# Performance work log

Measured on AMD Instinct MI355X. Metric: run time of the kernel, lower is better.

Reference implementation:

```python
import jax, jax.numpy as jnp
import numpy as np

IN_FEATURES = 4096
OUT_FEATURES = 4096
LORA_R = 64
LORA_ALPHA = 16
SCALING = LORA_ALPHA / LORA_R  # 0.25


def setup_inputs() -> dict:
    key = jax.random.key(0)
    k_x, k_w, k_s, k_a, k_b = jax.random.split(key, 5)
    x = jax.random.normal(k_x, (4, 2048, IN_FEATURES), dtype=jnp.float32)
    # int8 quantized base weight in [-8, 7] as in the torch buffer init
    weight_quantized = jax.random.randint(k_w, (OUT_FEATURES, IN_FEATURES), -8, 7, dtype=jnp.int8)
    weight_scale = jax.random.normal(k_s, (1,), dtype=jnp.float32)
    lora_A = jax.random.normal(k_a, (LORA_R, IN_FEATURES), dtype=jnp.float32) * 0.01
    # torch init is zeros; use small random values so the LoRA path is exercised
    lora_B = jax.random.normal(k_b, (OUT_FEATURES, LORA_R), dtype=jnp.float32) * 0.01
    return {"x": x, "weight_quantized": weight_quantized, "weight_scale": weight_scale,
            "lora_A": lora_A, "lora_B": lora_B}


def reference(x, weight_quantized, weight_scale, lora_A, lora_B):
    # 1. dequantize base weight on the fly: [out, in]
    w_dequant = weight_quantized.astype(x.dtype) * weight_scale
    # 2. base GEMM: [B, S, in] x [in, out] -> [B, S, out]
    base = jnp.einsum('bsi,oi->bso', x, w_dequant)
    # 3. LoRA low-rank update (dropout is identity in eval mode)
    lora = jnp.einsum('bsr,or->bso', jnp.einsum('bsi,ri->bsr', x, lora_A), lora_B)
    return base + lora * SCALING
```

## Files before the change

### kernel.cpp

```cpp
#include <hip/hip_runtime.h>

#define M_TOT 8192
#define K_TOT 4096
#define N_TOT 4096
#define RANK  64
#define SCALING 0.25f

typedef __bf16 bf16x8 __attribute__((ext_vector_type(8)));
typedef float floatx4 __attribute__((ext_vector_type(4)));

static __device__ __forceinline__ unsigned short f32_to_bf16(float f) {
  unsigned int u = __float_as_uint(f);
  u += 0x7FFFu + ((u >> 16) & 1u);
  return (unsigned short)(u >> 16);
}

static __device__ __forceinline__ void async_ld16(const void* g, void* l) {
  __builtin_amdgcn_global_load_lds(
      (const __attribute__((address_space(1))) unsigned int*)g,
      (__attribute__((address_space(3))) unsigned int*)l, 16, 0, 0);
}

__global__ __launch_bounds__(256) void cvt_x_kernel(const float4* __restrict__ x,
                                                    ushort4* __restrict__ xb) {
  int i = blockIdx.x * 256 + threadIdx.x;
  float4 v = x[i];
  ushort4 o;
  o.x = f32_to_bf16(v.x);
  o.y = f32_to_bf16(v.y);
  o.z = f32_to_bf16(v.z);
  o.w = f32_to_bf16(v.w);
  xb[i] = o;
}

__global__ __launch_bounds__(256) void build_weff_kernel(
    const int* __restrict__ wq, const float* __restrict__ scale_p,
    const float* __restrict__ A, const float* __restrict__ B,
    unsigned short* __restrict__ Weff) {
  __shared__ float Bs[64][65];
  __shared__ float As[64][65];

  const int tid = threadIdx.x;
  const int o0 = blockIdx.y * 64;
  const int k0 = blockIdx.x * 64;
  const float scale = scale_p[0];

  for (int i = tid; i < 64 * 64; i += 256) {
    int o = i >> 6, r = i & 63;
    Bs[o][r] = B[(size_t)(o0 + o) * RANK + r];
  }
  for (int i = tid; i < 64 * 64; i += 256) {
    int r = i >> 6, kk = i & 63;
    As[r][kk] = A[(size_t)r * K_TOT + k0 + kk];
  }
  __syncthreads();

  const int to = tid >> 4;
  const int tk = tid & 15;
  float acc[4][4] = {};
#pragma unroll 8
  for (int r = 0; r < RANK; ++r) {
    float bv[4], av[4];
#pragma unroll
    for (int a = 0; a < 4; ++a) bv[a] = Bs[to * 4 + a][r];
#pragma unroll
    for (int b = 0; b < 4; ++b) av[b] = As[r][tk * 4 + b];
#pragma unroll
    for (int a = 0; a < 4; ++a)
#pragma unroll
      for (int b = 0; b < 4; ++b) acc[a][b] += bv[a] * av[b];
  }
#pragma unroll
  for (int a = 0; a < 4; ++a) {
    const int o = o0 + to * 4 + a;
    const size_t base = (size_t)o * K_TOT + k0 + tk * 4;
    const int4 wv = *(const int4*)(wq + base);
    ushort4 st;
    st.x = f32_to_bf16((float)wv.x * scale + SCALING * acc[a][0]);
    st.y = f32_to_bf16((float)wv.y * scale + SCALING * acc[a][1]);
    st.z = f32_to_bf16((float)wv.z * scale + SCALING * acc[a][2]);
    st.w = f32_to_bf16((float)wv.w * scale + SCALING * acc[a][3]);
    *(ushort4*)(Weff + base) = st;
  }
}

__global__ __launch_bounds__(256) void gemm_kernel(
    const unsigned short* __restrict__ Xb,
    const unsigned short* __restrict__ Wb,
    float* __restrict__ out) {
  __shared__ __align__(16) unsigned short As[2 * 128 * 32];
  __shared__ __align__(16) unsigned short Bs[2 * 128 * 32];

  const int tid = threadIdx.x;
  const int lane = tid & 63;
  const int wave = tid >> 6;
  const int wm = wave >> 1;
  const int wn = wave & 1;

  const int bM = blockIdx.y * 128;
  const int bN = blockIdx.x * 128;

  const int sRow = tid >> 2;
  const int sCol = (tid & 3) * 8;
  const unsigned short* xg0 = Xb + (size_t)(bM + sRow) * K_TOT + sCol;
  const unsigned short* xg1 = xg0 + (size_t)64 * K_TOT;
  const unsigned short* wg0 = Wb + (size_t)(bN + sRow) * K_TOT + sCol;
  const unsigned short* wg1 = wg0 + (size_t)64 * K_TOT;
  unsigned short* la00 = As + tid * 8;
  unsigned short* la01 = As + 64 * 32 + tid * 8;
  unsigned short* la10 = As + 128 * 32 + tid * 8;
  unsigned short* la11 = As + 128 * 32 + 64 * 32 + tid * 8;
  unsigned short* lb00 = Bs + tid * 8;
  unsigned short* lb01 = Bs + 64 * 32 + tid * 8;
  unsigned short* lb10 = Bs + 128 * 32 + tid * 8;
  unsigned short* lb11 = Bs + 128 * 32 + 64 * 32 + tid * 8;

  const unsigned short* pa = As + ((wm * 64) + (lane & 15)) * 32 + (lane >> 4) * 8;
  const unsigned short* pb = Bs + ((wn * 64) + (lane & 15)) * 32 + (lane >> 4) * 8;

  floatx4 acc[4][4] = {};

  for (int kt = 0; kt < K_TOT; kt += 64) {
    __syncthreads();
    async_ld16(xg0 + kt, la00);
    async_ld16(xg1 + kt, la01);
    async_ld16(xg0 + kt + 32, la10);
    async_ld16(xg1 + kt + 32, la11);
    async_ld16(wg0 + kt, lb00);
    async_ld16(wg1 + kt, lb01);
    async_ld16(wg0 + kt + 32, lb10);
    async_ld16(wg1 + kt + 32, lb11);
    __syncthreads();

#pragma unroll
    for (int ks = 0; ks < 2; ++ks) {
      const unsigned short* pak = pa + ks * 128 * 32;
      const unsigned short* pbk = pb + ks * 128 * 32;
      bf16x8 af[4], bf[4];
#pragma unroll
      for (int i = 0; i < 4; ++i) af[i] = *(const bf16x8*)(pak + i * 16 * 32);
#pragma unroll
      for (int j = 0; j < 4; ++j) bf[j] = *(const bf16x8*)(pbk + j * 16 * 32);
#pragma unroll
      for (int i = 0; i < 4; ++i)
#pragma unroll
        for (int j = 0; j < 4; ++j)
          acc[i][j] = __builtin_amdgcn_mfma_f32_16x16x32_bf16(af[i], bf[j], acc[i][j], 0, 0, 0);
    }
  }

  const int row0 = bM + wm * 64 + ((lane >> 4) << 2);
  const int col0 = bN + wn * 64 + (lane & 15);
#pragma unroll
  for (int i = 0; i < 4; ++i) {
#pragma unroll
    for (int j = 0; j < 4; ++j) {
#pragma unroll
      for (int r = 0; r < 4; ++r) {
        out[(size_t)(row0 + i * 16 + r) * N_TOT + (col0 + j * 16)] = acc[i][j][r];
      }
    }
  }
}

extern "C" void kernel_launch(void* const* d_in, const int* in_sizes, int n_in,
                              void* d_out, int out_size, void* d_ws, size_t ws_size,
                              hipStream_t stream) {
  const float* x      = (const float*)d_in[0];
  const int*   wq     = (const int*)d_in[1];
  const float* wscale = (const float*)d_in[2];
  const float* lora_A = (const float*)d_in[3];
  const float* lora_B = (const float*)d_in[4];
  float* out = (float*)d_out;

  unsigned short* xb   = (unsigned short*)d_ws;
  unsigned short* weff = (unsigned short*)((char*)d_ws + (size_t)M_TOT * K_TOT * 2);

  cvt_x_kernel<<<32768, 256, 0, stream>>>((const float4*)x, (ushort4*)xb);
  build_weff_kernel<<<dim3(K_TOT / 64, N_TOT / 64), 256, 0, stream>>>(
      wq, wscale, lora_A, lora_B, weff);
  gemm_kernel<<<dim3(N_TOT / 128, M_TOT / 128), 256, 0, stream>>>(xb, weff, out);
}
```

Baseline: 596.3 us.

## Compute LoRA as separate low-rank path instead of folding into dequantized weight

The LoRA update is no longer folded into a dense effective weight through a scalar-FMA B@A product. A prep kernel now dequantizes the weight and converts A and the pre-scaled B to bf16. A new MFMA kernel computes Y = X·Aᵀ, and the main GEMM adds one extra K=64 step of Y·Bᵀ before writing out. This removes the dense rank-64 outer-product work per weight element, but adds a second full pass over X in a kernel launched with only 128 blocks, which may be latency bound.

```diff
diff --git a/kernel.cpp b/kernel.cpp
--- a/kernel.cpp
+++ b/kernel.cpp
@@ -33,60 +33,100 @@
   xb[i] = o;
 }
 
-__global__ __launch_bounds__(256) void build_weff_kernel(
+__global__ __launch_bounds__(256) void prep_kernel(
     const int* __restrict__ wq, const float* __restrict__ scale_p,
     const float* __restrict__ A, const float* __restrict__ B,
-    unsigned short* __restrict__ Weff) {
-  __shared__ float Bs[64][65];
-  __shared__ float As[64][65];
-
+    unsigned short* __restrict__ Weff, unsigned short* __restrict__ Ab,
+    unsigned short* __restrict__ Bb) {
+  const int blk = blockIdx.x;
   const int tid = threadIdx.x;
-  const int o0 = blockIdx.y * 64;
-  const int k0 = blockIdx.x * 64;
-  const float scale = scale_p[0];
-
-  for (int i = tid; i < 64 * 64; i += 256) {
-    int o = i >> 6, r = i & 63;
-    Bs[o][r] = B[(size_t)(o0 + o) * RANK + r];
-  }
-  for (int i = tid; i < 64 * 64; i += 256) {
-    int r = i >> 6, kk = i & 63;
-    As[r][kk] = A[(size_t)r * K_TOT + k0 + kk];
-  }
-  __syncthreads();
-
-  const int to = tid >> 4;
-  const int tk = tid & 15;
-  float acc[4][4] = {};
-#pragma unroll 8
-  for (int r = 0; r < RANK; ++r) {
-    float bv[4], av[4];
-#pragma unroll
-    for (int a = 0; a < 4; ++a) bv[a] = Bs[to * 4 + a][r];
-#pragma unroll
-    for (int b = 0; b < 4; ++b) av[b] = As[r][tk * 4 + b];
-#pragma unroll
-    for (int a = 0; a < 4; ++a)
-#pragma unroll
-      for (int b = 0; b < 4; ++b) acc[a][b] += bv[a] * av[b];
-  }
-#pragma unroll
-  for (int a = 0; a < 4; ++a) {
-    const int o = o0 + to * 4 + a;
-    const size_t base = (size_t)o * K_TOT + k0 + tk * 4;
-    const int4 wv = *(const int4*)(wq + base);
+  if (blk < 16384) {
+    const float scale = scale_p[0];
+    const size_t i = (size_t)(blk * 256 + tid) * 4;
+    const int4 wv = *(const int4*)(wq + i);
     ushort4 st;
-    st.x = f32_to_bf16((float)wv.x * scale + SCALING * acc[a][0]);
-    st.y = f32_to_bf16((float)wv.y * scale + SCALING * acc[a][1]);
-    st.z = f32_to_bf16((float)wv.z * scale + SCALING * acc[a][2]);
-    st.w = f32_to_bf16((float)wv.w * scale + SCALING * acc[a][3]);
-    *(ushort4*)(Weff + base) = st;
-  }
+    st.x = f32_to_bf16((float)wv.x * scale);
+    st.y = f32_to_bf16((float)wv.y * scale);
+    st.z = f32_to_bf16((float)wv.z * scale);
+    st.w = f32_to_bf16((float)wv.w * scale);
+    *(ushort4*)(Weff + i) = st;
+  } else if (blk < 16640) {
+    const size_t i = (size_t)((blk - 16384) * 256 + tid) * 4;
+    const float4 v = *(const float4*)(A + i);
+    ushort4 st;
+    st.x = f32_to_bf16(v.x);
+    st.y = f32_to_bf16(v.y);
+    st.z = f32_to_bf16(v.z);
+    st.w = f32_to_bf16(v.w);
+    *(ushort4*)(Ab + i) = st;
+  } else {
+    const size_t i = (size_t)((blk - 16640) * 256 + tid) * 4;
+    const float4 v = *(const float4*)(B + i);
+    ushort4 st;
+    st.x = f32_to_bf16(v.x * SCALING);
+    st.y = f32_to_bf16(v.y * SCALING);
+    st.z = f32_to_bf16(v.z * SCALING);
+    st.w = f32_to_bf16(v.w * SCALING);
+    *(ushort4*)(Bb + i) = st;
+  }
+}
+
+__global__ __launch_bounds__(256) void lora_y_kernel(
+    const unsigned short* __restrict__ Xb,
+    const unsigned short* __restrict__ Ab,
+    unsigned short* __restrict__ Yb) {
+  __shared__ __align__(16) unsigned short Xs[2 * 64 * 32];
+  __shared__ __align__(16) unsigned short As[2 * 64 * 32];
+
+  const int tid = threadIdx.x;
+  const int lane = tid & 63;
+  const int wave = tid >> 6;
+  const int m0 = blockIdx.x * 64;
+
+  const int sRow = tid >> 2;
+  const int sCol = (tid & 3) * 8;
+  const unsigned short* xg = Xb + (size_t)(m0 + sRow) * K_TOT + sCol;
+  const unsigned short* ag = Ab + (size_t)sRow * K_TOT + sCol;
+  unsigned short* lx0 = Xs + tid * 8;
+  unsigned short* lx1 = Xs + 64 * 32 + tid * 8;
+  unsigned short* la0 = As + tid * 8;
+  unsigned short* la1 = As + 64 * 32 + tid * 8;
+
+  const unsigned short* px = Xs + (wave * 16 + (lane & 15)) * 32 + (lane >> 4) * 8;
+  const unsigned short* pav = As + (lane & 15) * 32 + (lane >> 4) * 8;
+
+  floatx4 acc[4] = {};
+  for (int kt = 0; kt < K_TOT; kt += 64) {
+    __syncthreads();
+    async_ld16(xg + kt, lx0);
+    async_ld16(xg + kt + 32, lx1);
+    async_ld16(ag + kt, la0);
+    async_ld16(ag + kt + 32, la1);
+    __syncthreads();
+#pragma unroll
+    for (int ks = 0; ks < 2; ++ks) {
+      bf16x8 xf = *(const bf16x8*)(px + ks * 64 * 32);
+#pragma unroll
+      for (int j = 0; j < 4; ++j) {
+        bf16x8 af = *(const bf16x8*)(pav + ks * 64 * 32 + j * 16 * 32);
+        acc[j] = __builtin_amdgcn_mfma_f32_16x16x32_bf16(xf, af, acc[j], 0, 0, 0);
+      }
+    }
+  }
+  const int row0 = m0 + wave * 16 + ((lane >> 4) << 2);
+  const int col0 = lane & 15;
+#pragma unroll
+  for (int j = 0; j < 4; ++j)
+#pragma unroll
+    for (int r = 0; r < 4; ++r)
+      Yb[(size_t)(row0 + r) * RANK + (col0 + j * 16)] = f32_to_bf16(acc[j][r]);
 }
 
 __global__ __launch_bounds__(256) void gemm_kernel(
     const unsigned short* __restrict__ Xb,
     const unsigned short* __restrict__ Wb,
+    const unsigned short* __restrict__ Yb,
+    const unsigned short* __restrict__ Bb,
     float* __restrict__ out) {
   __shared__ __align__(16) unsigned short As[2 * 128 * 32];
   __shared__ __align__(16) unsigned short Bs[2 * 128 * 32];
@@ -149,18 +189,47 @@
     }
   }
 
+  {
+    const unsigned short* yg0 = Yb + (size_t)(bM + sRow) * RANK + sCol;
+    const unsigned short* yg1 = yg0 + (size_t)64 * RANK;
+    const unsigned short* bg0 = Bb + (size_t)(bN + sRow) * RANK + sCol;
+    const unsigned short* bg1 = bg0 + (size_t)64 * RANK;
+    __syncthreads();
+    async_ld16(yg0, la00);
+    async_ld16(yg1, la01);
+    async_ld16(yg0 + 32, la10);
+    async_ld16(yg1 + 32, la11);
+    async_ld16(bg0, lb00);
+    async_ld16(bg1, lb01);
+    async_ld16(bg0 + 32, lb10);
+    async_ld16(bg1 + 32, lb11);
+    __syncthreads();
+#pragma unroll
+    for (int ks = 0; ks < 2; ++ks) {
+      const unsigned short* pak = pa + ks * 128 * 32;
+      const unsigned short* pbk = pb + ks * 128 * 32;
+      bf16x8 af[4], bf[4];
+#pragma unroll
+      for (int i = 0; i < 4; ++i) af[i] = *(const bf16x8*)(pak + i * 16 * 32);
+#pragma unroll
+      for (int j = 0; j < 4; ++j) bf[j] = *(const bf16x8*)(pbk + j * 16 * 32);
+#pragma unroll
+      for (int i = 0; i < 4; ++i)
+#pragma unroll
+        for (int j = 0; j < 4; ++j)
+          acc[i][j] = __builtin_amdgcn_mfma_f32_16x16x32_bf16(af[i], bf[j], acc[i][j], 0, 0, 0);
+    }
+  }
+
   const int row0 = bM + wm * 64 + ((lane >> 4) << 2);
   const int col0 = bN + wn * 64 + (lane & 15);
 #pragma unroll
-  for (int i = 0; i < 4; ++i) {
-#pragma unroll
-    for (int j = 0; j < 4; ++j) {
-#pragma unroll
-      for (int r = 0; r < 4; ++r) {
+  for (int i = 0; i < 4; ++i)
+#pragma unroll
+    for (int j = 0; j < 4; ++j)
+#pragma unroll
+      for (int r = 0; r < 4; ++r)
         out[(size_t)(row0 + i * 16 + r) * N_TOT + (col0 + j * 16)] = acc[i][j][r];
-      }
-    }
-  }
 }
 
 extern "C" void kernel_launch(void* const* d_in, const int* in_sizes, int n_in,
@@ -173,11 +242,15 @@
   const float* lora_B = (const float*)d_in[4];
   float* out = (float*)d_out;
 
-  unsigned short* xb   = (unsigned short*)d_ws;
-  unsigned short* weff = (unsigned short*)((char*)d_ws + (size_t)M_TOT * K_TOT * 2);
+  char* ws = (char*)d_ws;
+  unsigned short* xb   = (unsigned short*)(ws);
+  unsigned short* weff = (unsigned short*)(ws + 67108864);
+  unsigned short* yb   = (unsigned short*)(ws + 100663296);
+  unsigned short* ab   = (unsigned short*)(ws + 101711872);
+  unsigned short* bb   = (unsigned short*)(ws + 102236160);
 
   cvt_x_kernel<<<32768, 256, 0, stream>>>((const float4*)x, (ushort4*)xb);
-  build_weff_kernel<<<dim3(K_TOT / 64, N_TOT / 64), 256, 0, stream>>>(
-      wq, wscale, lora_A, lora_B, weff);
-  gemm_kernel<<<dim3(N_TOT / 128, M_TOT / 128), 256, 0, stream>>>(xb, weff, out);
-}
+  prep_kernel<<<16896, 256, 0, stream>>>(wq, wscale, lora_A, lora_B, weff, ab, bb);
+  lora_y_kernel<<<128, 256, 0, stream>>>(xb, ab, yb);
+  gemm_kernel<<<dim3(N_TOT / 128, M_TOT / 128), 256, 0, stream>>>(xb, weff, yb, bb, out);
+}
```

New measurement: 606.2 us. About the same (+1.7%).
